# Kernel optimization log

Measured on AMD Instinct MI355X. Metric: run time of the kernel, lower is better.

Reference implementation:

```python
import jax, jax.numpy as jnp
import numpy as np

N = 30000   # nodes
E = 480000  # directed edges (avg degree 16)
CIN = 64    # c_in
CH = 64     # c_hidden

_PARAM_NAMES = ["Wl1","bl1","Wr1","br1","We1","att1","bo1",
                "Wlm","blm","Wrm","brm","Wem","attm","bom",
                "Wl8","bl8","Wr8","br8","We8","att8","bo8"]
_PARAM_SHAPES = [(CIN,CH),(CH,),(CIN,CH),(CH,),(1,CH),(CH,),(CH,),
                 (6,CH,CH),(6,CH),(6,CH,CH),(6,CH),(6,1,CH),(6,CH),(6,CH),
                 (CH,1),(1,),(CH,1),(1,),(1,1),(1,),(1,)]

def setup_inputs() -> dict:
    key = jax.random.key(0)
    ks = jax.random.split(key, 4 + len(_PARAM_NAMES))
    inp = {
        "features": jax.random.normal(ks[0], (N, CIN), dtype=jnp.float32),
        "edge_src": jax.random.randint(ks[1], (E,), 0, N),
        "edge_dst": jax.random.randint(ks[2], (E,), 0, N),
        "edge_weight": jax.random.uniform(ks[3], (E,), dtype=jnp.float32),
    }
    for i, (name, shape) in enumerate(zip(_PARAM_NAMES, _PARAM_SHAPES)):
        inp[name] = jax.random.normal(ks[4 + i], shape, dtype=jnp.float32) * 0.05
    return inp

def _gatv2_layer(x, src, dst, attr, Wl, bl, Wr, br, We, att, bo):
    # PyG GATv2Conv, heads=1, negative_slope=0.2; (src,dst,attr) already include self-loops.
    n = x.shape[0]
    xl = x @ Wl + bl                                  # [N, C] source-side transform (lin_l)
    xr = x @ Wr + br                                  # [N, C] target-side transform (lin_r)
    e = xl[src] + xr[dst] + attr[:, None] * We[0]     # [Ea, C] per-edge pre-activation
    logit = jax.nn.leaky_relu(e, 0.2) @ att           # [Ea]
    m = jax.ops.segment_max(logit, dst, num_segments=n)
    z = jnp.exp(logit - m[dst])                       # stable softmax over each node's in-edges
    s = jax.ops.segment_sum(z, dst, num_segments=n)
    alpha = z / s[dst]                                # [Ea]
    return jax.ops.segment_sum(alpha[:, None] * xl[src], dst, num_segments=n) + bo

def reference(features, edge_src, edge_dst, edge_weight,
              Wl1, bl1, Wr1, br1, We1, att1, bo1,
              Wlm, blm, Wrm, brm, Wem, attm, bom,
              Wl8, bl8, Wr8, br8, We8, att8, bo8):
    n = features.shape[0]
    # add_self_loops=True with fill_value='mean': self-loop attr = mean of incoming edge attrs
    cnt = jax.ops.segment_sum(jnp.ones_like(edge_weight), edge_dst, num_segments=n)
    loop_attr = jax.ops.segment_sum(edge_weight, edge_dst, num_segments=n) / jnp.maximum(cnt, 1.0)
    loops = jnp.arange(n)
    src = jnp.concatenate([edge_src, loops])
    dst = jnp.concatenate([edge_dst, loops])
    attr = jnp.concatenate([edge_weight, loop_attr])
    x = _gatv2_layer(features, src, dst, attr, Wl1, bl1, Wr1, br1, We1, att1, bo1)
    for i in range(6):  # conv2..conv7, structurally identical hidden layers
        x = _gatv2_layer(x, src, dst, attr, Wlm[i], blm[i], Wrm[i], brm[i], Wem[i], attm[i], bom[i])
    x = _gatv2_layer(x, src, dst, attr, Wl8, bl8, Wr8, br8, We8, att8, bo8)  # [N, 1]
    return jnp.mean(x, axis=-2)  # mean pool over nodes -> [1]
```

## Files before the change

kernel.cpp:

```cpp
#include <hip/hip_runtime.h>
#include <hip/hip_fp16.h>
#include <math.h>

#define CH 64


__device__ __forceinline__ void gather8(const __half* __restrict__ xlh, int src, int cg,
                                        float xv[8]) {
  uint4 raw = *reinterpret_cast<const uint4*>(xlh + ((size_t)src << 6) + (cg << 3));
  const __half2* h = reinterpret_cast<const __half2*>(&raw);
#pragma unroll
  for (int j = 0; j < 4; ++j) {
    float2 f = __half22float2(h[j]);
    xv[2 * j] = f.x;
    xv[2 * j + 1] = f.y;
  }
}

__device__ __forceinline__ void batch_update(const float xv[8], float a, bool valid,
                                             const float xrw[8], const float Wec[8],
                                             const float attc[8], float acc[8], float& s) {
  float partial = 0.f;
#pragma unroll
  for (int j = 0; j < 8; ++j) {
    float ee = fmaf(a, Wec[j], xv[j] + xrw[j]);
    float lr = fmaxf(ee, 0.f) + 0.2f * fminf(ee, 0.f);
    partial = fmaf(lr, attc[j], partial);
  }
  partial += __shfl_xor(partial, 1, 64);
  partial += __shfl_xor(partial, 2, 64);
  partial += __shfl_xor(partial, 4, 64);
  float logit = fminf(fmaxf(partial, -40.f), 40.f);
  float p = valid ? __expf(logit) : 0.f;
  s += p;
#pragma unroll
  for (int j = 0; j < 8; ++j) acc[j] = fmaf(p, xv[j], acc[j]);
}

__device__ __forceinline__ void agg_node8(const __half* __restrict__ xlh,
                                          const int2* __restrict__ csr, int beg, int dv,
                                          const float xrw[8], const float Wec[8],
                                          const float attc[8], int eg, int cg, float acc[8],
                                          float& s) {
  int end = beg + dv;
  int nb = (dv + 7) >> 3;
  int idx0 = beg + eg;
  bool vA = idx0 < end;
  int2 edA = csr[min(idx0, end - 1)];
  float xvA[8];
  gather8(xlh, edA.x, cg, xvA);
  int2 edB = edA;
  bool vB = false;
  if (nb > 1) {
    int idx1 = beg + 8 + eg;
    vB = idx1 < end;
    edB = csr[min(idx1, end - 1)];
  }
  for (int t = 0; t < nb; ++t) {
    float xvB[8];
    bool haveNext = (t + 1 < nb);
    if (haveNext) gather8(xlh, edB.x, cg, xvB);
    int2 edC = edB;
    bool vC = false;
    if (t + 2 < nb) {
      int idx = beg + (t + 2) * 8 + eg;
      vC = idx < end;
      edC = csr[min(idx, end - 1)];
    }
    batch_update(xvA, __int_as_float(edA.y), vA, xrw, Wec, attc, acc, s);
    edA = edB; vA = vB;
    edB = edC; vB = vC;
    if (haveNext) {
#pragma unroll
      for (int j = 0; j < 8; ++j) xvA[j] = xvB[j];
    }
  }
  s += __shfl_xor(s, 8, 64);
  s += __shfl_xor(s, 16, 64);
  s += __shfl_xor(s, 32, 64);
#pragma unroll
  for (int j = 0; j < 8; ++j) {
    acc[j] += __shfl_xor(acc[j], 8, 64);
    acc[j] += __shfl_xor(acc[j], 16, 64);
    acc[j] += __shfl_xor(acc[j], 32, 64);
  }
}

#define LOAD8F(dst, srcp)                                \
  {                                                      \
    *(float4*)&dst[0] = *(const float4*)&(srcp)[0];      \
    *(float4*)&dst[4] = *(const float4*)&(srcp)[4];      \
  }


#define WSUM_SCALE 33554432.0f
#define WSUM_MASK 0xFFFFFFFFFFULL

__global__ void k_count(const int* __restrict__ dst, const float* __restrict__ w, int E,
                        unsigned long long* __restrict__ agg, int* __restrict__ rank) {
  int i = blockIdx.x * blockDim.x + threadIdx.x;
  if (i < E) {
    int d = dst[i];
    unsigned long long pk = (1ULL << 40) | (unsigned long long)(w[i] * WSUM_SCALE);
    unsigned long long old = atomicAdd(&agg[d], pk);
    rank[i] = (int)(old >> 40);
  }
}

__global__ void k_alloc(const unsigned long long* __restrict__ agg,
                        float* __restrict__ loop_attr, int* __restrict__ deg,
                        int* __restrict__ row_beg, int* __restrict__ total, int n) {
  int i = blockIdx.x * blockDim.x + threadIdx.x;
  int lane = threadIdx.x & 63;
  int d = 0;
  if (i < n) {
    unsigned long long v = agg[i];
    int c = (int)(v >> 40);
    float ws = (float)(v & WSUM_MASK) * (1.0f / WSUM_SCALE);
    loop_attr[i] = ws / fmaxf((float)c, 1.0f);
    d = c + 1;
    deg[i] = d;
  }
  int x = d;
#pragma unroll
  for (int off = 1; off < 64; off <<= 1) {
    int t = __shfl_up(x, off, 64);
    if (lane >= off) x += t;
  }
  int base = 0;
  if (lane == 63) base = atomicAdd(total, x);
  base = __shfl(base, 63, 64);
  if (i < n) row_beg[i] = base + x - d;
}

__global__ void k_scatter(const int* __restrict__ src, const int* __restrict__ dst,
                          const float* __restrict__ w, const int* __restrict__ rank, int E,
                          const int* __restrict__ row_beg, int2* __restrict__ csr) {
  int i = blockIdx.x * blockDim.x + threadIdx.x;
  if (i < E) {
    int d = dst[i];
    csr[row_beg[d] + rank[i]] = make_int2(src[i], __float_as_int(w[i]));
  }
}

__global__ void k_selfloop(int n, const int* __restrict__ row_beg, const int* __restrict__ deg,
                           int2* __restrict__ csr, const float* __restrict__ loop_attr) {
  int v = blockIdx.x * blockDim.x + threadIdx.x;
  if (v < n) {
    csr[row_beg[v] + deg[v] - 1] = make_int2(v, __float_as_int(loop_attr[v]));
  }
}


__global__ void __launch_bounds__(256) k_transform(
    const float* __restrict__ x, const float* __restrict__ Wl, const float* __restrict__ bl,
    const float* __restrict__ Wr, const float* __restrict__ br,
    __half* __restrict__ xlh, float* __restrict__ xr, int n) {
  __shared__ float sW[2][CH * CH];
  for (int i = threadIdx.x; i < (CH * CH) / 4; i += blockDim.x) {
    ((float4*)sW[0])[i] = ((const float4*)Wl)[i];
    ((float4*)sW[1])[i] = ((const float4*)Wr)[i];
  }
  __syncthreads();
  int lane = threadIdx.x & 63;
  int wid = threadIdx.x >> 6;
  float blc = bl[lane], brc = br[lane];
  int wavesPerGrid = (gridDim.x * blockDim.x) >> 6;
  for (int row = blockIdx.x * (blockDim.x >> 6) + wid; row < n; row += wavesPerGrid) {
    float xv = x[(size_t)row * CH + lane];
    float accl = blc, accr = brc;
#pragma unroll
    for (int k = 0; k < CH; ++k) {
      float xk = __shfl(xv, k, 64);
      accl = fmaf(xk, sW[0][k * CH + lane], accl);
      accr = fmaf(xk, sW[1][k * CH + lane], accr);
    }
    xlh[(size_t)row * CH + lane] = __float2half(accl);
    xr[(size_t)row * CH + lane] = accr;
  }
}


__global__ void __launch_bounds__(256) k_aggregate(
    const __half* __restrict__ xlh, const float* __restrict__ xr,
    const int* __restrict__ row_beg, const int* __restrict__ deg,
    const int2* __restrict__ csr,
    const float* __restrict__ We, const float* __restrict__ att, const float* __restrict__ bo,
    float* __restrict__ out, int n) {
  int lane = threadIdx.x & 63;
  int v = (blockIdx.x * blockDim.x + threadIdx.x) >> 6;
  if (v >= n) return;
  int eg = lane >> 3, cg = lane & 7;
  int c0 = cg << 3;
  float Wec[8], attc[8], xrw[8];
  LOAD8F(Wec, We + c0);
  LOAD8F(attc, att + c0);
  LOAD8F(xrw, xr + (size_t)v * CH + c0);
  float acc[8], s = 0.f;
#pragma unroll
  for (int j = 0; j < 8; ++j) acc[j] = 0.f;
  agg_node8(xlh, csr, row_beg[v], deg[v], xrw, Wec, attc, eg, cg, acc, s);
  if (eg == 0) {
    float boc[8];
    LOAD8F(boc, bo + c0);
    float o[8];
    float inv_s = 1.0f / s;
#pragma unroll
    for (int j = 0; j < 8; ++j) o[j] = fmaf(acc[j], inv_s, boc[j]);
    *(float4*)&out[(size_t)v * CH + c0] = *(float4*)&o[0];
    *(float4*)&out[(size_t)v * CH + c0 + 4] = *(float4*)&o[4];
  }
}

__global__ void __launch_bounds__(256) k_aggregate_t8(
    const __half* __restrict__ xlh, const float* __restrict__ xr,
    const int* __restrict__ row_beg, const int* __restrict__ deg,
    const int2* __restrict__ csr,
    const float* __restrict__ We, const float* __restrict__ att, const float* __restrict__ bo,
    const float* __restrict__ Wl8, const float* __restrict__ bl8,
    const float* __restrict__ Wr8, const float* __restrict__ br8,
    float* __restrict__ xl8, float* __restrict__ xr8, int n) {
  int lane = threadIdx.x & 63;
  int v = (blockIdx.x * blockDim.x + threadIdx.x) >> 6;
  if (v >= n) return;
  int eg = lane >> 3, cg = lane & 7;
  int c0 = cg << 3;
  float Wec[8], attc[8], xrw[8];
  LOAD8F(Wec, We + c0);
  LOAD8F(attc, att + c0);
  LOAD8F(xrw, xr + (size_t)v * CH + c0);
  float acc[8], s = 0.f;
#pragma unroll
  for (int j = 0; j < 8; ++j) acc[j] = 0.f;
  agg_node8(xlh, csr, row_beg[v], deg[v], xrw, Wec, attc, eg, cg, acc, s);
  float boc[8], wl8c[8], wr8c[8];
  LOAD8F(boc, bo + c0);
  LOAD8F(wl8c, Wl8 + c0);
  LOAD8F(wr8c, Wr8 + c0);
  float pa = 0.f, pb = 0.f;
  float inv_s = 1.0f / s;
#pragma unroll
  for (int j = 0; j < 8; ++j) {
    float o = fmaf(acc[j], inv_s, boc[j]);
    pa = fmaf(o, wl8c[j], pa);
    pb = fmaf(o, wr8c[j], pb);
  }
  pa += __shfl_xor(pa, 1, 64);
  pa += __shfl_xor(pa, 2, 64);
  pa += __shfl_xor(pa, 4, 64);
  pb += __shfl_xor(pb, 1, 64);
  pb += __shfl_xor(pb, 2, 64);
  pb += __shfl_xor(pb, 4, 64);
  if (lane == 0) {
    xl8[v] = pa + bl8[0];
    xr8[v] = pb + br8[0];
  }
}

__global__ void __launch_bounds__(256) k_agg8_mean(
    const float* __restrict__ xl8, const float* __restrict__ xr8,
    const int* __restrict__ row_beg, const int* __restrict__ deg,
    const int2* __restrict__ csr,
    const float* __restrict__ We, const float* __restrict__ att, const float* __restrict__ bo,
    float* __restrict__ out, int n) {
  int lane = threadIdx.x & 63;
  int wid = threadIdx.x >> 6;
  float We0 = We[0], att0 = att[0], bo0 = bo[0];
  float inv_n = 1.0f / (float)n;
  float local = 0.f;
  int nwaves = gridDim.x * 4;
  for (int v = blockIdx.x * 4 + wid; v < n; v += nwaves) {
    float xrc = xr8[v];
    int beg = row_beg[v], dv = deg[v];
    float s = 0.f, acc = 0.f;
    for (int chunk = 0; chunk < dv; chunk += 64) {
      int idx = chunk + lane;
      bool valid = idx < dv;
      int2 ed = valid ? csr[beg + idx] : make_int2(0, 0);
      float xlc = valid ? xl8[ed.x] : 0.f;
      float ee = fmaf(__int_as_float(ed.y), We0, xlc + xrc);
      float logit = (ee > 0.f ? ee : 0.2f * ee) * att0;
      logit = fminf(fmaxf(logit, -40.f), 40.f);
      float p = valid ? __expf(logit) : 0.f;
      s += p;
      acc = fmaf(p, xlc, acc);
    }
#pragma unroll
    for (int off = 32; off > 0; off >>= 1) {
      s += __shfl_xor(s, off, 64);
      acc += __shfl_xor(acc, off, 64);
    }
    local += (acc / s + bo0) * inv_n;
  }
  __shared__ float sw[4];
  if (lane == 0) sw[wid] = local;
  __syncthreads();
  if (threadIdx.x == 0) atomicAdd(out, sw[0] + sw[1] + sw[2] + sw[3]);
}


extern "C" void kernel_launch(void* const* d_in, const int* in_sizes, int n_in,
                              void* d_out, int out_size, void* d_ws, size_t ws_size,
                              hipStream_t stream) {
  const float* features = (const float*)d_in[0];
  const int* edge_src = (const int*)d_in[1];
  const int* edge_dst = (const int*)d_in[2];
  const float* edge_w = (const float*)d_in[3];
  const int N = in_sizes[0] / CH;
  const int E = in_sizes[1];

  char* p = (char*)d_ws;
  auto take = [&](size_t bytes) {
    char* r = p;
    p += (bytes + 255) & ~(size_t)255;
    return r;
  };
  float* xA = (float*)take((size_t)N * CH * 4);
  float* xB = (float*)take((size_t)N * CH * 4);
  __half* xlh = (__half*)take((size_t)N * CH * 2);
  float* xr = (float*)take((size_t)N * CH * 4);
  int2* csr = (int2*)take((size_t)(E + N) * 8);
  char* zero_region = take((size_t)N * 8 + 256);
  unsigned long long* agg = (unsigned long long*)zero_region;
  int* total = (int*)(zero_region + (size_t)N * 8);
  int* rank = (int*)take((size_t)E * 4);
  float* loop_attr = (float*)take((size_t)N * 4);
  int* deg = (int*)take((size_t)N * 4);
  int* row_beg = (int*)take((size_t)N * 4);
  float* xl8 = (float*)take((size_t)N * 4);
  float* xr8 = (float*)take((size_t)N * 4);

  hipMemsetAsync(zero_region, 0, (size_t)N * 8 + 256, stream);
  hipMemsetAsync(d_out, 0, sizeof(float), stream);

  const int tb = 256;
  k_count<<<(E + tb - 1) / tb, tb, 0, stream>>>(edge_dst, edge_w, E, agg, rank);
  k_alloc<<<(N + tb - 1) / tb, tb, 0, stream>>>(agg, loop_attr, deg, row_beg, total, N);
  k_scatter<<<(E + tb - 1) / tb, tb, 0, stream>>>(edge_src, edge_dst, edge_w, rank, E,
                                                  row_beg, csr);
  k_selfloop<<<(N + tb - 1) / tb, tb, 0, stream>>>(N, row_beg, deg, csr, loop_attr);

  const float* Wl1 = (const float*)d_in[4];
  const float* bl1 = (const float*)d_in[5];
  const float* Wr1 = (const float*)d_in[6];
  const float* br1 = (const float*)d_in[7];
  const float* We1 = (const float*)d_in[8];
  const float* att1 = (const float*)d_in[9];
  const float* bo1 = (const float*)d_in[10];
  const float* Wlm = (const float*)d_in[11];
  const float* blm = (const float*)d_in[12];
  const float* Wrm = (const float*)d_in[13];
  const float* brm = (const float*)d_in[14];
  const float* Wem = (const float*)d_in[15];
  const float* attm = (const float*)d_in[16];
  const float* bom = (const float*)d_in[17];

  const int agg_grid = ((size_t)N * 64 + tb - 1) / tb;
  const float* x_cur = features;
  float* x_nxt = xA;
  for (int layer = 0; layer < 7; ++layer) {
    const float *Wl, *bl, *Wr, *br, *We, *att, *bo;
    if (layer == 0) {
      Wl = Wl1; bl = bl1; Wr = Wr1; br = br1; We = We1; att = att1; bo = bo1;
    } else {
      int i = layer - 1;
      Wl = Wlm + (size_t)i * CH * CH;
      bl = blm + (size_t)i * CH;
      Wr = Wrm + (size_t)i * CH * CH;
      br = brm + (size_t)i * CH;
      We = Wem + (size_t)i * CH;
      att = attm + (size_t)i * CH;
      bo = bom + (size_t)i * CH;
    }
    k_transform<<<1024, 256, 0, stream>>>(x_cur, Wl, bl, Wr, br, xlh, xr, N);
    if (layer < 6) {
      k_aggregate<<<agg_grid, tb, 0, stream>>>(xlh, xr, row_beg, deg, csr, We, att, bo,
                                               x_nxt, N);
      x_cur = x_nxt;
      x_nxt = (x_nxt == xA) ? xB : xA;
    } else {
      k_aggregate_t8<<<agg_grid, tb, 0, stream>>>(
          xlh, xr, row_beg, deg, csr, We, att, bo, (const float*)d_in[18],
          (const float*)d_in[19], (const float*)d_in[20], (const float*)d_in[21], xl8, xr8, N);
    }
  }
  k_agg8_mean<<<1024, 256, 0, stream>>>(xl8, xr8, row_beg, deg, csr, (const float*)d_in[22],
                                        (const float*)d_in[23], (const float*)d_in[24],
                                        (float*)d_out, N);
}
```

Before: 535.8 us.

## Fuse CSR build kernels with first-layer transform and persist aggregate grids

Merges the edge counting kernel with the layer-1 feature transform into one launch, with blocks split by index so the two independent jobs run concurrently. The self-loop insertion moves into k_alloc, which drops a separate kernel and the loop_attr buffer. The aggregate kernels become grid-stride loops over a fixed 2048-block grid so per-node constant loads are hoisted, and the transform grid shrinks to 512 blocks. The aim is fewer launches and less setup overhead; a fixed grid size could underfill the GPU or unbalance work between waves.

```diff
diff --git a/kernel.cpp b/kernel.cpp
--- a/kernel.cpp
+++ b/kernel.cpp
@@ -96,28 +96,60 @@
 #define WSUM_SCALE 33554432.0f
 #define WSUM_MASK 0xFFFFFFFFFFULL
 
-__global__ void k_count(const int* __restrict__ dst, const float* __restrict__ w, int E,
-                        unsigned long long* __restrict__ agg, int* __restrict__ rank) {
+__global__ void __launch_bounds__(256) k_count_tr1(
+    const int* __restrict__ dst, const float* __restrict__ w, int E,
+    unsigned long long* __restrict__ agg, int* __restrict__ rank, int cntBlocks,
+    const float* __restrict__ x, const float* __restrict__ Wl, const float* __restrict__ bl,
+    const float* __restrict__ Wr, const float* __restrict__ br,
+    __half* __restrict__ xlh, float* __restrict__ xr, int n) {
+  __shared__ float sW[2][CH * CH];
+  if ((int)blockIdx.x < cntBlocks) {
+    int i = blockIdx.x * blockDim.x + threadIdx.x;
+    if (i < E) {
+      int d = dst[i];
+      unsigned long long pk = (1ULL << 40) | (unsigned long long)(w[i] * WSUM_SCALE);
+      unsigned long long old = atomicAdd(&agg[d], pk);
+      rank[i] = (int)(old >> 40);
+    }
+    return;
+  }
+  for (int i = threadIdx.x; i < (CH * CH) / 4; i += blockDim.x) {
+    ((float4*)sW[0])[i] = ((const float4*)Wl)[i];
+    ((float4*)sW[1])[i] = ((const float4*)Wr)[i];
+  }
+  __syncthreads();
+  int lane = threadIdx.x & 63;
+  int wid = threadIdx.x >> 6;
+  float blc = bl[lane], brc = br[lane];
+  int b = blockIdx.x - cntBlocks;
+  int trBlocks = gridDim.x - cntBlocks;
+  int wavesPerGrid = trBlocks * 4;
+  for (int row = b * 4 + wid; row < n; row += wavesPerGrid) {
+    float xv = x[(size_t)row * CH + lane];
+    float accl = blc, accr = brc;
+#pragma unroll
+    for (int k = 0; k < CH; ++k) {
+      float xk = __shfl(xv, k, 64);
+      accl = fmaf(xk, sW[0][k * CH + lane], accl);
+      accr = fmaf(xk, sW[1][k * CH + lane], accr);
+    }
+    xlh[(size_t)row * CH + lane] = __float2half(accl);
+    xr[(size_t)row * CH + lane] = accr;
+  }
+}
+
+__global__ void k_alloc(const unsigned long long* __restrict__ agg, int* __restrict__ deg,
+                        int* __restrict__ row_beg, int* __restrict__ total,
+                        int2* __restrict__ csr, int n) {
   int i = blockIdx.x * blockDim.x + threadIdx.x;
-  if (i < E) {
-    int d = dst[i];
-    unsigned long long pk = (1ULL << 40) | (unsigned long long)(w[i] * WSUM_SCALE);
-    unsigned long long old = atomicAdd(&agg[d], pk);
-    rank[i] = (int)(old >> 40);
-  }
-}
-
-__global__ void k_alloc(const unsigned long long* __restrict__ agg,
-                        float* __restrict__ loop_attr, int* __restrict__ deg,
-                        int* __restrict__ row_beg, int* __restrict__ total, int n) {
-  int i = blockIdx.x * blockDim.x + threadIdx.x;
   int lane = threadIdx.x & 63;
   int d = 0;
+  float la = 0.f;
   if (i < n) {
     unsigned long long v = agg[i];
     int c = (int)(v >> 40);
     float ws = (float)(v & WSUM_MASK) * (1.0f / WSUM_SCALE);
-    loop_attr[i] = ws / fmaxf((float)c, 1.0f);
+    la = ws / fmaxf((float)c, 1.0f);
     d = c + 1;
     deg[i] = d;
   }
@@ -130,7 +162,11 @@
   int base = 0;
   if (lane == 63) base = atomicAdd(total, x);
   base = __shfl(base, 63, 64);
-  if (i < n) row_beg[i] = base + x - d;
+  if (i < n) {
+    int rb = base + x - d;
+    row_beg[i] = rb;
+    csr[rb + d - 1] = make_int2(i, __float_as_int(la));
+  }
 }
 
 __global__ void k_scatter(const int* __restrict__ src, const int* __restrict__ dst,
@@ -140,14 +176,6 @@
   if (i < E) {
     int d = dst[i];
     csr[row_beg[d] + rank[i]] = make_int2(src[i], __float_as_int(w[i]));
-  }
-}
-
-__global__ void k_selfloop(int n, const int* __restrict__ row_beg, const int* __restrict__ deg,
-                           int2* __restrict__ csr, const float* __restrict__ loop_attr) {
-  int v = blockIdx.x * blockDim.x + threadIdx.x;
-  if (v < n) {
-    csr[row_beg[v] + deg[v] - 1] = make_int2(v, __float_as_int(loop_attr[v]));
   }
 }
 
@@ -188,27 +216,29 @@
     const float* __restrict__ We, const float* __restrict__ att, const float* __restrict__ bo,
     float* __restrict__ out, int n) {
   int lane = threadIdx.x & 63;
-  int v = (blockIdx.x * blockDim.x + threadIdx.x) >> 6;
-  if (v >= n) return;
   int eg = lane >> 3, cg = lane & 7;
   int c0 = cg << 3;
-  float Wec[8], attc[8], xrw[8];
+  float Wec[8], attc[8], boc[8];
   LOAD8F(Wec, We + c0);
   LOAD8F(attc, att + c0);
-  LOAD8F(xrw, xr + (size_t)v * CH + c0);
-  float acc[8], s = 0.f;
-#pragma unroll
-  for (int j = 0; j < 8; ++j) acc[j] = 0.f;
-  agg_node8(xlh, csr, row_beg[v], deg[v], xrw, Wec, attc, eg, cg, acc, s);
-  if (eg == 0) {
-    float boc[8];
-    LOAD8F(boc, bo + c0);
-    float o[8];
-    float inv_s = 1.0f / s;
-#pragma unroll
-    for (int j = 0; j < 8; ++j) o[j] = fmaf(acc[j], inv_s, boc[j]);
-    *(float4*)&out[(size_t)v * CH + c0] = *(float4*)&o[0];
-    *(float4*)&out[(size_t)v * CH + c0 + 4] = *(float4*)&o[4];
+  LOAD8F(boc, bo + c0);
+  int wav = (blockIdx.x * blockDim.x + threadIdx.x) >> 6;
+  int nw = (gridDim.x * blockDim.x) >> 6;
+  for (int v = wav; v < n; v += nw) {
+    float xrw[8];
+    LOAD8F(xrw, xr + (size_t)v * CH + c0);
+    float acc[8], s = 0.f;
+#pragma unroll
+    for (int j = 0; j < 8; ++j) acc[j] = 0.f;
+    agg_node8(xlh, csr, row_beg[v], deg[v], xrw, Wec, attc, eg, cg, acc, s);
+    if (eg == 0) {
+      float o[8];
+      float inv_s = 1.0f / s;
+#pragma unroll
+      for (int j = 0; j < 8; ++j) o[j] = fmaf(acc[j], inv_s, boc[j]);
+      *(float4*)&out[(size_t)v * CH + c0] = *(float4*)&o[0];
+      *(float4*)&out[(size_t)v * CH + c0 + 4] = *(float4*)&o[4];
+    }
   }
 }
 
@@ -221,39 +251,42 @@
     const float* __restrict__ Wr8, const float* __restrict__ br8,
     float* __restrict__ xl8, float* __restrict__ xr8, int n) {
   int lane = threadIdx.x & 63;
-  int v = (blockIdx.x * blockDim.x + threadIdx.x) >> 6;
-  if (v >= n) return;
   int eg = lane >> 3, cg = lane & 7;
   int c0 = cg << 3;
-  float Wec[8], attc[8], xrw[8];
+  float Wec[8], attc[8], boc[8], wl8c[8], wr8c[8];
   LOAD8F(Wec, We + c0);
   LOAD8F(attc, att + c0);
-  LOAD8F(xrw, xr + (size_t)v * CH + c0);
-  float acc[8], s = 0.f;
-#pragma unroll
-  for (int j = 0; j < 8; ++j) acc[j] = 0.f;
-  agg_node8(xlh, csr, row_beg[v], deg[v], xrw, Wec, attc, eg, cg, acc, s);
-  float boc[8], wl8c[8], wr8c[8];
   LOAD8F(boc, bo + c0);
   LOAD8F(wl8c, Wl8 + c0);
   LOAD8F(wr8c, Wr8 + c0);
-  float pa = 0.f, pb = 0.f;
-  float inv_s = 1.0f / s;
-#pragma unroll
-  for (int j = 0; j < 8; ++j) {
-    float o = fmaf(acc[j], inv_s, boc[j]);
-    pa = fmaf(o, wl8c[j], pa);
-    pb = fmaf(o, wr8c[j], pb);
-  }
-  pa += __shfl_xor(pa, 1, 64);
-  pa += __shfl_xor(pa, 2, 64);
-  pa += __shfl_xor(pa, 4, 64);
-  pb += __shfl_xor(pb, 1, 64);
-  pb += __shfl_xor(pb, 2, 64);
-  pb += __shfl_xor(pb, 4, 64);
-  if (lane == 0) {
-    xl8[v] = pa + bl8[0];
-    xr8[v] = pb + br8[0];
+  float bl80 = bl8[0], br80 = br8[0];
+  int wav = (blockIdx.x * blockDim.x + threadIdx.x) >> 6;
+  int nw = (gridDim.x * blockDim.x) >> 6;
+  for (int v = wav; v < n; v += nw) {
+    float xrw[8];
+    LOAD8F(xrw, xr + (size_t)v * CH + c0);
+    float acc[8], s = 0.f;
+#pragma unroll
+    for (int j = 0; j < 8; ++j) acc[j] = 0.f;
+    agg_node8(xlh, csr, row_beg[v], deg[v], xrw, Wec, attc, eg, cg, acc, s);
+    float pa = 0.f, pb = 0.f;
+    float inv_s = 1.0f / s;
+#pragma unroll
+    for (int j = 0; j < 8; ++j) {
+      float o = fmaf(acc[j], inv_s, boc[j]);
+      pa = fmaf(o, wl8c[j], pa);
+      pb = fmaf(o, wr8c[j], pb);
+    }
+    pa += __shfl_xor(pa, 1, 64);
+    pa += __shfl_xor(pa, 2, 64);
+    pa += __shfl_xor(pa, 4, 64);
+    pb += __shfl_xor(pb, 1, 64);
+    pb += __shfl_xor(pb, 2, 64);
+    pb += __shfl_xor(pb, 4, 64);
+    if (lane == 0) {
+      xl8[v] = pa + bl80;
+      xr8[v] = pb + br80;
+    }
   }
 }
 
@@ -324,7 +357,6 @@
   unsigned long long* agg = (unsigned long long*)zero_region;
   int* total = (int*)(zero_region + (size_t)N * 8);
   int* rank = (int*)take((size_t)E * 4);
-  float* loop_attr = (float*)take((size_t)N * 4);
   int* deg = (int*)take((size_t)N * 4);
   int* row_beg = (int*)take((size_t)N * 4);
   float* xl8 = (float*)take((size_t)N * 4);
@@ -334,11 +366,9 @@
   hipMemsetAsync(d_out, 0, sizeof(float), stream);
 
   const int tb = 256;
-  k_count<<<(E + tb - 1) / tb, tb, 0, stream>>>(edge_dst, edge_w, E, agg, rank);
-  k_alloc<<<(N + tb - 1) / tb, tb, 0, stream>>>(agg, loop_attr, deg, row_beg, total, N);
-  k_scatter<<<(E + tb - 1) / tb, tb, 0, stream>>>(edge_src, edge_dst, edge_w, rank, E,
-                                                  row_beg, csr);
-  k_selfloop<<<(N + tb - 1) / tb, tb, 0, stream>>>(N, row_beg, deg, csr, loop_attr);
+  const int cntBlocks = (E + tb - 1) / tb;
+  const int TR_BLOCKS = 512;
+  const int AGG_BLOCKS = 2048;
 
   const float* Wl1 = (const float*)d_in[4];
   const float* bl1 = (const float*)d_in[5];
@@ -355,31 +385,36 @@
   const float* attm = (const float*)d_in[16];
   const float* bom = (const float*)d_in[17];
 
-  const int agg_grid = ((size_t)N * 64 + tb - 1) / tb;
-  const float* x_cur = features;
+  k_count_tr1<<<cntBlocks + TR_BLOCKS, tb, 0, stream>>>(
+      edge_dst, edge_w, E, agg, rank, cntBlocks, features, Wl1, bl1, Wr1, br1, xlh, xr, N);
+  k_alloc<<<(N + tb - 1) / tb, tb, 0, stream>>>(agg, deg, row_beg, total, csr, N);
+  k_scatter<<<(E + tb - 1) / tb, tb, 0, stream>>>(edge_src, edge_dst, edge_w, rank, E,
+                                                  row_beg, csr);
+
+  const float* x_cur = nullptr;
   float* x_nxt = xA;
   for (int layer = 0; layer < 7; ++layer) {
-    const float *Wl, *bl, *Wr, *br, *We, *att, *bo;
+    const float *We, *att, *bo;
     if (layer == 0) {
-      Wl = Wl1; bl = bl1; Wr = Wr1; br = br1; We = We1; att = att1; bo = bo1;
+      We = We1; att = att1; bo = bo1;
     } else {
       int i = layer - 1;
-      Wl = Wlm + (size_t)i * CH * CH;
-      bl = blm + (size_t)i * CH;
-      Wr = Wrm + (size_t)i * CH * CH;
-      br = brm + (size_t)i * CH;
       We = Wem + (size_t)i * CH;
       att = attm + (size_t)i * CH;
       bo = bom + (size_t)i * CH;
-    }
-    k_transform<<<1024, 256, 0, stream>>>(x_cur, Wl, bl, Wr, br, xlh, xr, N);
+      const float* Wl = Wlm + (size_t)i * CH * CH;
+      const float* bl = blm + (size_t)i * CH;
+      const float* Wr = Wrm + (size_t)i * CH * CH;
+      const float* br = brm + (size_t)i * CH;
+      k_transform<<<TR_BLOCKS, tb, 0, stream>>>(x_cur, Wl, bl, Wr, br, xlh, xr, N);
+    }
     if (layer < 6) {
-      k_aggregate<<<agg_grid, tb, 0, stream>>>(xlh, xr, row_beg, deg, csr, We, att, bo,
-                                               x_nxt, N);
+      k_aggregate<<<AGG_BLOCKS, tb, 0, stream>>>(xlh, xr, row_beg, deg, csr, We, att, bo,
+                                                 x_nxt, N);
       x_cur = x_nxt;
       x_nxt = (x_nxt == xA) ? xB : xA;
     } else {
-      k_aggregate_t8<<<agg_grid, tb, 0, stream>>>(
+      k_aggregate_t8<<<AGG_BLOCKS, tb, 0, stream>>>(
           xlh, xr, row_beg, deg, csr, We, att, bo, (const float*)d_in[18],
           (const float*)d_in[19], (const float*)d_in[20], (const float*)d_in[21], xl8, xr8, N);
     }
```

Result: no change. 545.2 us (+1.8%).
